# Kernel optimization log

Hardware: AMD Instinct MI355X
Metric: run time of the kernel (lower is better)

Reference implementation:

```python
import jax, jax.numpy as jnp
import numpy as np

N, S, E = 32768, 64, 256  # n_nodes, seq_len (== features_dim), n_edges


def setup_inputs() -> dict:
    key = jax.random.key(0)
    ks = jax.random.split(key, 8)
    inputs = jax.random.normal(ks[0], (N, S, S), dtype=jnp.float32)
    input_masks = jax.random.randint(ks[1], (N, S), 0, 2, dtype=jnp.int32)
    edge_index = jax.random.randint(ks[2], (2, E), 0, N, dtype=jnp.int32)
    sc = 1.0 / np.sqrt(S).astype(np.float32)
    Wq = jax.random.normal(ks[3], (S, S), dtype=jnp.float32) * sc
    Wk = jax.random.normal(ks[4], (S, S), dtype=jnp.float32) * sc
    wv = jax.random.normal(ks[5], (S,), dtype=jnp.float32) * sc
    Wfc = jax.random.normal(ks[6], (S, 2 * S), dtype=jnp.float32) * (1.0 / np.sqrt(2 * S).astype(np.float32))
    bfc = jax.random.normal(ks[7], (S,), dtype=jnp.float32) * 0.01
    return {"inputs": inputs, "input_masks": input_masks, "edge_index": edge_index,
            "Wq": Wq, "Wk": Wk, "wv": wv, "Wfc": Wfc, "bfc": bfc}


def reference(inputs, input_masks, edge_index, Wq, Wk, wv, Wfc, bfc):
    # valid length per node = number of unmasked sequence positions
    valid = jnp.sum(input_masks, axis=1)  # [N] int
    pos = jnp.arange(S)                   # key positions

    def atten(q_in, kv, vlen):
        # d2l-style additive attention (eval mode, dropout off).
        # q_in, kv: [S, S];  vlen: scalar valid length over key axis.
        q = q_in @ Wq.T                                    # [S, H]
        k = kv @ Wk.T                                      # [S, H]
        feats = jnp.tanh(q[:, None, :] + k[None, :, :])    # [Sq, Sk, H]
        scores = jnp.einsum('qkh,h->qk', feats, wv)        # [Sq, Sk]
        scores = jnp.where(pos[None, :] < vlen, scores, -1e6)
        w = jax.nn.softmax(scores, axis=-1)
        return w @ kv                                      # [S, S]

    def step(emb, edge):
        x, y = edge[0], edge[1]
        ex, ey = emb[x], emb[y]                            # [S, S] each
        y2x = atten(ex, ey, valid[x])
        x2y = atten(ey, ex, valid[y])
        # fc(cat(a,b,dim=0).T).T  ==  Wfc @ cat(a,b,axis=0) + bfc[:,None]
        x_out = Wfc @ jnp.concatenate([ex, y2x], axis=0) + bfc[:, None]
        y_out = Wfc @ jnp.concatenate([ey, x2y], axis=0) + bfc[:, None]
        emb = emb.at[x].set(x_out).at[y].set(y_out)
        return emb, None

    out, _ = jax.lax.scan(step, inputs, edge_index.T)  # sequential edge loop
    return out
```

## Files before the change

### kernel.cpp

```cpp
#include <hip/hip_runtime.h>

#define S 64
#define ST 68
#define STW 132
#define E_EDGES 256
#define NT 512
#define N_NODES 32768
#define NPB 128
#define NPAIRS 64

typedef float vf4 __attribute__((ext_vector_type(4)));

__device__ __forceinline__ float v_rcp(float x) {
  float r;
  asm("v_rcp_f32 %0, %1" : "=v"(r) : "v"(x));
  return r;
}

__device__ __forceinline__ float tanh_term(float x) {
  float t = __builtin_amdgcn_exp2f(x * 2.88539008177793f);
  return fmaf(-2.0f, v_rcp(t + 1.0f), 1.0f);
}

__global__ void init_kernel(const int* __restrict__ edges, int* __restrict__ done,
                            unsigned int* __restrict__ bitmap) {
  const int tid = threadIdx.x;
  if (tid < E_EDGES) done[tid] = 0;
  bitmap[tid] = 0u;
  __syncthreads();
  if (tid < 2 * E_EDGES) {
    int node = edges[tid];
    atomicOr(&bitmap[node >> 5], 1u << (node & 31));
  }
}

__global__ __launch_bounds__(NT, 1) void fused_kernel(
    const float* __restrict__ inputs,
    const int* __restrict__ masks,
    const int* __restrict__ edges,
    const float* __restrict__ Wq,
    const float* __restrict__ Wk,
    const float* __restrict__ wv,
    const float* __restrict__ Wfc,
    const float* __restrict__ bfc,
    float* __restrict__ out,
    int* __restrict__ done,
    const unsigned int* __restrict__ bitmap) {
  const int tid = threadIdx.x;
  const int e = blockIdx.x;
  const int lane = tid & 63;
  const int wvid = tid >> 6;

  __shared__ float sWqT[S][ST];
  __shared__ float sWkT[S][ST];
  __shared__ float sWfc[S][STW];
  __shared__ float sEx[S][ST];
  __shared__ float sEy[S][ST];
  __shared__ float sQ[S][ST];
  __shared__ float sK[S][ST];
  __shared__ float sP[S][ST];
  __shared__ float swv[S];
  __shared__ float sbfc[S];
  __shared__ unsigned int sBitmap[N_NODES / 32];
  __shared__ int sMeta[6];

  const int a = edges[e];
  const int b = edges[E_EDGES + e];

  if (tid < 2) sMeta[tid] = -1;
  __syncthreads();
  if (tid < e) {
    int xa = edges[tid], yb = edges[E_EDGES + tid];
    if (xa == a || yb == a) atomicMax(&sMeta[0], tid);
    if (xa == b || yb == b) atomicMax(&sMeta[1], tid);
  }

#pragma unroll
  for (int k = 0; k < 2; ++k) {
    int i4 = tid + k * NT;
    int h = i4 >> 4, j0 = (i4 & 15) << 2;
    float4 q4 = *(const float4*)(Wq + h * S + j0);
    float4 k4 = *(const float4*)(Wk + h * S + j0);
    sWqT[j0 + 0][h] = q4.x; sWqT[j0 + 1][h] = q4.y;
    sWqT[j0 + 2][h] = q4.z; sWqT[j0 + 3][h] = q4.w;
    sWkT[j0 + 0][h] = k4.x; sWkT[j0 + 1][h] = k4.y;
    sWkT[j0 + 2][h] = k4.z; sWkT[j0 + 3][h] = k4.w;
  }
#pragma unroll
  for (int k = 0; k < 4; ++k) {
    int i4 = tid + k * NT;
    int h = i4 >> 5, r0 = (i4 & 31) << 2;
    *(float4*)&sWfc[h][r0] = *(const float4*)(Wfc + h * 2 * S + r0);
  }
  if (tid < S) { swv[tid] = wv[tid]; sbfc[tid] = bfc[tid]; }
  sBitmap[tid] = bitmap[tid];
  sBitmap[tid + NT] = bitmap[tid + NT];

  int mv = 0;
  if (wvid == 0) mv = masks[(size_t)a * S + lane];
  else if (wvid == 1) mv = masks[(size_t)b * S + lane];
#pragma unroll
  for (int d = 1; d < 64; d <<= 1) mv += __shfl_xor(mv, d, 64);
  if (tid == 0) sMeta[2] = mv;
  if (tid == 64) sMeta[3] = mv;

  __syncthreads();
  const int depA = sMeta[0], depB = sMeta[1];
  const int validA = sMeta[2], validB = sMeta[3];

  auto copy_pair = [&](int p) {
    const int n0 = e * NPB + 2 * p;
    const int n1 = n0 + 1;
    const size_t f4 = (size_t)n0 * 1024;
    const vf4* __restrict__ src = (const vf4*)inputs + f4;
    vf4* __restrict__ dst = (vf4*)out + f4;
    vf4 v0 = __builtin_nontemporal_load(src + tid);
    vf4 v1 = __builtin_nontemporal_load(src + tid + 512);
    vf4 v2 = __builtin_nontemporal_load(src + tid + 1024);
    vf4 v3 = __builtin_nontemporal_load(src + tid + 1536);
    if (!(sBitmap[n0 >> 5] & (1u << (n0 & 31)))) {
      __builtin_nontemporal_store(v0, dst + tid);
      __builtin_nontemporal_store(v1, dst + tid + 512);
    }
    if (!(sBitmap[n1 >> 5] & (1u << (n1 & 31)))) {
      __builtin_nontemporal_store(v2, dst + tid + 1024);
      __builtin_nontemporal_store(v3, dst + tid + 1536);
    }
  };

  int g = 0;
  auto cp2 = [&]() {
    if (g < NPAIRS) {
      copy_pair(g);
      copy_pair(g + 1);
      g += 2;
    }
  };

  if (depA >= 0 || depB >= 0) {
    for (;;) {
      __syncthreads();
      if (tid == 0) {
        int ok = 1;
        if (depA >= 0 &&
            __hip_atomic_load(&done[depA], __ATOMIC_RELAXED, __HIP_MEMORY_SCOPE_AGENT) == 0)
          ok = 0;
        if (ok && depB >= 0 &&
            __hip_atomic_load(&done[depB], __ATOMIC_RELAXED, __HIP_MEMORY_SCOPE_AGENT) == 0)
          ok = 0;
        sMeta[4] = ok;
      }
      __syncthreads();
      if (sMeta[4]) break;
      if (g < NPAIRS) {
        copy_pair(g);
        copy_pair(g + 1);
        g += 2;
      } else {
        __builtin_amdgcn_s_sleep(16);
      }
    }
    if (tid == 0) {
      if (depA >= 0)
        (void)__hip_atomic_load(&done[depA], __ATOMIC_ACQUIRE, __HIP_MEMORY_SCOPE_AGENT);
      if (depB >= 0)
        (void)__hip_atomic_load(&done[depB], __ATOMIC_ACQUIRE, __HIP_MEMORY_SCOPE_AGENT);
    }
    __syncthreads();
  }

  const float* exg = (depA >= 0) ? out + (size_t)a * 4096 : inputs + (size_t)a * 4096;
  const float* eyg = (depB >= 0) ? out + (size_t)b * 4096 : inputs + (size_t)b * 4096;
#pragma unroll
  for (int k = 0; k < 2; ++k) {
    int i4 = tid + k * NT;
    int r = i4 >> 4, c4 = (i4 & 15) << 2;
    *(float4*)&sEx[r][c4] = *(const float4*)(exg + r * S + c4);
    *(float4*)&sEy[r][c4] = *(const float4*)(eyg + r * S + c4);
  }
  __syncthreads();

  const int ty = tid >> 4;
  const int tx = tid & 15;
  const int c0 = tx << 2;

  auto proj = [&](const float (*A)[ST], const float (*WT)[ST], float (*D)[ST]) {
    float acc[2][4] = {};
#pragma unroll 4
    for (int j0 = 0; j0 < S; j0 += 4) {
      float4 av[2];
      av[0] = *(const float4*)&A[ty][j0];
      av[1] = *(const float4*)&A[ty + 32][j0];
#pragma unroll
      for (int jj = 0; jj < 4; ++jj) {
        float4 w4 = *(const float4*)&WT[j0 + jj][c0];
#pragma unroll
        for (int s = 0; s < 2; ++s) {
          float as = (&av[s].x)[jj];
          acc[s][0] = fmaf(as, w4.x, acc[s][0]);
          acc[s][1] = fmaf(as, w4.y, acc[s][1]);
          acc[s][2] = fmaf(as, w4.z, acc[s][2]);
          acc[s][3] = fmaf(as, w4.w, acc[s][3]);
        }
      }
    }
    *(float4*)&D[ty][c0] = make_float4(acc[0][0], acc[0][1], acc[0][2], acc[0][3]);
    *(float4*)&D[ty + 32][c0] = make_float4(acc[1][0], acc[1][1], acc[1][2], acc[1][3]);
  };

  auto score_phase = [&](int vlen) {
    if (vlen == 0) {
#pragma unroll
      for (int u = 0; u < 4; ++u) {
        sP[ty][tx + 16 * u] = 0.015625f;
        sP[ty + 32][tx + 16 * u] = 0.015625f;
      }
      return;
    }
    float acc[2][4] = {};
#pragma unroll 2
    for (int h0 = 0; h0 < S; h0 += 4) {
      float4 q4[2];
      q4[0] = *(const float4*)&sQ[ty][h0];
      q4[1] = *(const float4*)&sQ[ty + 32][h0];
      float4 wv4 = *(const float4*)&swv[h0];
#pragma unroll
      for (int u = 0; u < 4; ++u) {
        if (16 * u < vlen) {
          float4 k4 = *(const float4*)&sK[tx + 16 * u][h0];
#pragma unroll
          for (int jj = 0; jj < 4; ++jj) {
            float kk = (&k4.x)[jj];
            float wvh = (&wv4.x)[jj];
            acc[0][u] = fmaf(tanh_term((&q4[0].x)[jj] + kk), wvh, acc[0][u]);
            acc[1][u] = fmaf(tanh_term((&q4[1].x)[jj] + kk), wvh, acc[1][u]);
          }
        }
      }
    }
#pragma unroll
    for (int u = 0; u < 4; ++u) {
      int cu = tx + 16 * u;
      sP[ty][cu] = (cu < vlen) ? acc[0][u] : 0.0f;
      sP[ty + 32][cu] = (cu < vlen) ? acc[1][u] : 0.0f;
    }
  };

  auto softmax_phase = [&](int vlen) {
    if (vlen == 0) return;
    const int row = tid >> 3, sub = tid & 7;
    float m = -3.0e38f;
#pragma unroll
    for (int k = 0; k < 8; ++k) {
      int c = sub + 8 * k;
      if (c < vlen) m = fmaxf(m, sP[row][c]);
    }
#pragma unroll
    for (int d = 1; d < 8; d <<= 1) m = fmaxf(m, __shfl_xor(m, d, 8));
    float p[8];
    float sum = 0.f;
#pragma unroll
    for (int k = 0; k < 8; ++k) {
      int c = sub + 8 * k;
      if (c < vlen) {
        p[k] = __expf(sP[row][c] - m);
        sum += p[k];
      }
    }
#pragma unroll
    for (int d = 1; d < 8; d <<= 1) sum += __shfl_xor(sum, d, 8);
    float inv = 1.0f / sum;
#pragma unroll
    for (int k = 0; k < 8; ++k) {
      int c = sub + 8 * k;
      if (c < vlen) sP[row][c] = p[k] * inv;
    }
  };

  auto pv_phase = [&](const float (*V)[ST], float (*D)[ST], int vlen) {
    const int kEnd = (vlen == 0) ? S : ((vlen + 3) & ~3);
    float acc[2][4] = {};
    for (int k0 = 0; k0 < kEnd; k0 += 4) {
      float4 p4[2];
      p4[0] = *(const float4*)&sP[ty][k0];
      p4[1] = *(const float4*)&sP[ty + 32][k0];
#pragma unroll
      for (int kk = 0; kk < 4; ++kk) {
        float4 v4 = *(const float4*)&V[k0 + kk][c0];
#pragma unroll
        for (int s = 0; s < 2; ++s) {
          float ps = (&p4[s].x)[kk];
          acc[s][0] = fmaf(ps, v4.x, acc[s][0]);
          acc[s][1] = fmaf(ps, v4.y, acc[s][1]);
          acc[s][2] = fmaf(ps, v4.z, acc[s][2]);
          acc[s][3] = fmaf(ps, v4.w, acc[s][3]);
        }
      }
    }
    *(float4*)&D[ty][c0] = make_float4(acc[0][0], acc[0][1], acc[0][2], acc[0][3]);
    *(float4*)&D[ty + 32][c0] = make_float4(acc[1][0], acc[1][1], acc[1][2], acc[1][3]);
  };

  auto fc_phase = [&](const float (*E1)[ST], const float (*A1)[ST], float* outg) {
    float acc[2][4];
#pragma unroll
    for (int s = 0; s < 2; ++s) {
      float bv = sbfc[ty + 32 * s];
      acc[s][0] = bv; acc[s][1] = bv; acc[s][2] = bv; acc[s][3] = bv;
    }
#pragma unroll 2
    for (int r0 = 0; r0 < S; r0 += 4) {
      float4 w4[2];
      w4[0] = *(const float4*)&sWfc[ty][r0];
      w4[1] = *(const float4*)&sWfc[ty + 32][r0];
#pragma unroll
      for (int rr = 0; rr < 4; ++rr) {
        float4 e4 = *(const float4*)&E1[r0 + rr][c0];
#pragma unroll
        for (int s = 0; s < 2; ++s) {
          float ws = (&w4[s].x)[rr];
          acc[s][0] = fmaf(ws, e4.x, acc[s][0]);
          acc[s][1] = fmaf(ws, e4.y, acc[s][1]);
          acc[s][2] = fmaf(ws, e4.z, acc[s][2]);
          acc[s][3] = fmaf(ws, e4.w, acc[s][3]);
        }
      }
    }
#pragma unroll 2
    for (int r0 = 0; r0 < S; r0 += 4) {
      float4 w4[2];
      w4[0] = *(const float4*)&sWfc[ty][S + r0];
      w4[1] = *(const float4*)&sWfc[ty + 32][S + r0];
#pragma unroll
      for (int rr = 0; rr < 4; ++rr) {
        float4 e4 = *(const float4*)&A1[r0 + rr][c0];
#pragma unroll
        for (int s = 0; s < 2; ++s) {
          float ws = (&w4[s].x)[rr];
          acc[s][0] = fmaf(ws, e4.x, acc[s][0]);
          acc[s][1] = fmaf(ws, e4.y, acc[s][1]);
          acc[s][2] = fmaf(ws, e4.z, acc[s][2]);
          acc[s][3] = fmaf(ws, e4.w, acc[s][3]);
        }
      }
    }
    *(float4*)(outg + (size_t)ty * S + c0) =
        make_float4(acc[0][0], acc[0][1], acc[0][2], acc[0][3]);
    *(float4*)(outg + (size_t)(ty + 32) * S + c0) =
        make_float4(acc[1][0], acc[1][1], acc[1][2], acc[1][3]);
  };

  proj(sEx, sWqT, sQ);
  proj(sEy, sWkT, sK);
  cp2();
  cp2();
  cp2();
  __syncthreads();
  score_phase(validA);
  cp2();
  cp2();
  cp2();
  __syncthreads();
  softmax_phase(validA);
  cp2();
  cp2();
  cp2();
  __syncthreads();
  pv_phase(sEy, sQ, validA);
  cp2();
  cp2();
  cp2();
  __syncthreads();
  fc_phase(sEx, sQ, out + (size_t)a * 4096);
  cp2();
  __syncthreads();

  proj(sEy, sWqT, sQ);
  proj(sEx, sWkT, sK);
  cp2();
  cp2();
  cp2();
  __syncthreads();
  score_phase(validB);
  cp2();
  cp2();
  cp2();
  __syncthreads();
  softmax_phase(validB);
  cp2();
  cp2();
  cp2();
  __syncthreads();
  pv_phase(sEx, sQ, validB);
  cp2();
  cp2();
  cp2();
  __syncthreads();
  fc_phase(sEy, sQ, out + (size_t)b * 4096);

  __syncthreads();
  if (tid == 0)
    __hip_atomic_store(&done[e], 1, __ATOMIC_RELEASE, __HIP_MEMORY_SCOPE_AGENT);

  for (; g < NPAIRS; g += 2) {
    copy_pair(g);
    copy_pair(g + 1);
  }
}

extern "C" void kernel_launch(void* const* d_in, const int* in_sizes, int n_in,
                              void* d_out, int out_size, void* d_ws, size_t ws_size,
                              hipStream_t stream) {
  const float* inputs = (const float*)d_in[0];
  const int* masks = (const int*)d_in[1];
  const int* edges = (const int*)d_in[2];
  const float* Wq = (const float*)d_in[3];
  const float* Wk = (const float*)d_in[4];
  const float* wv = (const float*)d_in[5];
  const float* Wfc = (const float*)d_in[6];
  const float* bfc = (const float*)d_in[7];
  float* out = (float*)d_out;
  int* done = (int*)d_ws;
  unsigned int* bitmap = (unsigned int*)(done + E_EDGES);

  init_kernel<<<1, 1024, 0, stream>>>(edges, done, bitmap);
  fused_kernel<<<E_EDGES, NT, 0, stream>>>(inputs, masks, edges, Wq, Wk, wv, Wfc,
                                           bfc, out, done, bitmap);
}
```

Measured before the change: 237.9 us.

## Redistribute bulk copy work only to edge blocks with no downstream dependents

The init kernel now marks each edge that feeds a later edge and ranks the remaining leaf edges. The pass-through copy of untouched nodes is split evenly across only those leaf blocks, so blocks on the dependency chain no longer spend time copying. The spin-wait sleep interval is also halved. This relieves the critical path, but the leaf blocks take on larger copy loads and the init kernel gains a serial O(E^2) scan.

```diff
diff --git a/kernel.cpp b/kernel.cpp
--- a/kernel.cpp
+++ b/kernel.cpp
@@ -6,8 +6,7 @@
 #define E_EDGES 256
 #define NT 512
 #define N_NODES 32768
-#define NPB 128
-#define NPAIRS 64
+#define NPAIRS_TOTAL 16384
 
 typedef float vf4 __attribute__((ext_vector_type(4)));
 
@@ -23,14 +22,30 @@
 }
 
 __global__ void init_kernel(const int* __restrict__ edges, int* __restrict__ done,
-                            unsigned int* __restrict__ bitmap) {
+                            unsigned int* __restrict__ bitmap, int* __restrict__ rankv) {
   const int tid = threadIdx.x;
+  __shared__ int feed[E_EDGES];
   if (tid < E_EDGES) done[tid] = 0;
   bitmap[tid] = 0u;
   __syncthreads();
   if (tid < 2 * E_EDGES) {
     int node = edges[tid];
     atomicOr(&bitmap[node >> 5], 1u << (node & 31));
+  }
+  if (tid < E_EDGES) {
+    int a = edges[tid], b = edges[E_EDGES + tid];
+    int f = 0;
+    for (int t = tid + 1; t < E_EDGES; ++t) {
+      int xa = edges[t], yb = edges[E_EDGES + t];
+      if (xa == a || yb == a || xa == b || yb == b) { f = 1; break; }
+    }
+    feed[tid] = f;
+  }
+  __syncthreads();
+  if (tid == 0) {
+    int r = 0;
+    for (int i = 0; i < E_EDGES; ++i) rankv[i] = feed[i] ? -1 : r++;
+    rankv[E_EDGES] = r;
   }
 }
 
@@ -45,7 +60,8 @@
     const float* __restrict__ bfc,
     float* __restrict__ out,
     int* __restrict__ done,
-    const unsigned int* __restrict__ bitmap) {
+    const unsigned int* __restrict__ bitmap,
+    const int* __restrict__ rankv) {
   const int tid = threadIdx.x;
   const int e = blockIdx.x;
   const int lane = tid & 63;
@@ -108,8 +124,18 @@
   const int depA = sMeta[0], depB = sMeta[1];
   const int validA = sMeta[2], validB = sMeta[3];
 
+  const int rk = rankv[e];
+  const int R = rankv[E_EDGES];
+  int g, pEnd;
+  if (rk < 0) {
+    g = pEnd = 0;
+  } else {
+    g = (NPAIRS_TOTAL * rk) / R;
+    pEnd = (NPAIRS_TOTAL * (rk + 1)) / R;
+  }
+
   auto copy_pair = [&](int p) {
-    const int n0 = e * NPB + 2 * p;
+    const int n0 = 2 * p;
     const int n1 = n0 + 1;
     const size_t f4 = (size_t)n0 * 1024;
     const vf4* __restrict__ src = (const vf4*)inputs + f4;
@@ -128,11 +154,10 @@
     }
   };
 
-  int g = 0;
   auto cp2 = [&]() {
-    if (g < NPAIRS) {
+    if (g < pEnd) {
       copy_pair(g);
-      copy_pair(g + 1);
+      if (g + 1 < pEnd) copy_pair(g + 1);
       g += 2;
     }
   };
@@ -152,12 +177,12 @@
       }
       __syncthreads();
       if (sMeta[4]) break;
-      if (g < NPAIRS) {
+      if (g < pEnd) {
         copy_pair(g);
-        copy_pair(g + 1);
+        if (g + 1 < pEnd) copy_pair(g + 1);
         g += 2;
       } else {
-        __builtin_amdgcn_s_sleep(16);
+        __builtin_amdgcn_s_sleep(8);
       }
     }
     if (tid == 0) {
@@ -402,10 +427,7 @@
   if (tid == 0)
     __hip_atomic_store(&done[e], 1, __ATOMIC_RELEASE, __HIP_MEMORY_SCOPE_AGENT);
 
-  for (; g < NPAIRS; g += 2) {
-    copy_pair(g);
-    copy_pair(g + 1);
-  }
+  for (; g < pEnd; ++g) copy_pair(g);
 }
 
 extern "C" void kernel_launch(void* const* d_in, const int* in_sizes, int n_in,
@@ -422,8 +444,9 @@
   float* out = (float*)d_out;
   int* done = (int*)d_ws;
   unsigned int* bitmap = (unsigned int*)(done + E_EDGES);
-
-  init_kernel<<<1, 1024, 0, stream>>>(edges, done, bitmap);
+  int* rankv = (int*)(bitmap + N_NODES / 32);
+
+  init_kernel<<<1, 1024, 0, stream>>>(edges, done, bitmap, rankv);
   fused_kernel<<<E_EDGES, NT, 0, stream>>>(inputs, masks, edges, Wq, Wk, wv, Wfc,
-                                           bfc, out, done, bitmap);
+                                           bfc, out, done, bitmap, rankv);
 }
```

Result: slower. 263.9 us (+10.9%).
